# Performance work log

Hardware: AMD Instinct MI355X
Metric: run time of the kernel (lower is better)

Reference implementation:

```python
import jax, jax.numpy as jnp
import numpy as np


def setup_inputs() -> dict:
    key = jax.random.key(0)
    ks = jax.random.split(key, 10)
    B, L, H, E, D = 2, 2048, 16, 64, 64
    d_model = 512
    inp = {
        "queries": jax.random.normal(ks[0], (B, L, H, E), jnp.float32),
        "keys": jax.random.normal(ks[1], (B, L, H, E), jnp.float32),
        "values": jax.random.normal(ks[2], (B, L, H, D), jnp.float32),
        "raw_series": jax.random.normal(ks[3], (B, L, d_model), jnp.float32),
        # learned fusion MLP: Linear(d_model, d_model//2) -> ReLU -> Linear(d_model//2, 1)
        "w1": jax.random.normal(ks[4], (d_model, d_model // 2), jnp.float32) / np.sqrt(d_model),
        "b1": jnp.zeros((d_model // 2,), jnp.float32),
        "w2": jax.random.normal(ks[5], (d_model // 2, 1), jnp.float32) / np.sqrt(d_model // 2),
        "b2": jnp.zeros((1,), jnp.float32),
        # per-head trend scaling, init ones
        "alpha_trend": jnp.ones((H,), jnp.float32),
    }
    return inp


MOMENTUM_ALPHA = 1.0
MOMENTUM_K = 1


def reference(queries, keys, values, raw_series, w1, b1, w2, b2, alpha_trend):
    B, L, H, E = queries.shape
    scale = 1.0 / jnp.sqrt(jnp.asarray(E, queries.dtype))

    # ---- soft momentum bias ----
    # learned fusion: MLP over features -> scalar per position, [B, L]
    h = jax.nn.relu(raw_series @ w1 + b1)
    fused = (h @ w2 + b2)[..., 0]                       # [B, L]
    k = max(1, min(MOMENTUM_K, L - 1))
    momentum = fused[:, k:] - fused[:, :-k]              # [B, L-k]
    momentum = jnp.pad(momentum, ((0, 0), (k, 0)))       # left-pad zeros -> [B, L]
    diff = jnp.abs(momentum[:, :, None] - momentum[:, None, :])  # [B, L, L]
    soft_bias = -MOMENTUM_ALPHA * diff                   # [B, L, L]

    # ---- attention ----
    scores = jnp.einsum('blhe,bshe->bhls', queries, keys)  # [B, H, L, L]
    scores = scores + soft_bias[:, None, :, :] * alpha_trend[None, :, None, None]
    causal = jnp.triu(jnp.ones((L, L), bool), k=1)       # True above diagonal
    scores = jnp.where(causal[None, None], -jnp.inf, scores)
    A = jax.nn.softmax(scale * scores, axis=-1)          # [B, H, L, L]
    V = jnp.einsum('bhls,bshd->blhd', A, values)         # [B, L, H, D]
    return V
```

## Files before the change

### kernel.cpp

```cpp
#include <hip/hip_runtime.h>
#include <math.h>

#define B_ 2
#define L_ 2048
#define H_ 16
#define E_ 64
#define D_ 64
#define DM_ 512
#define DH_ 256

typedef __bf16 bf16_t;
typedef bf16_t bf16x8_t __attribute__((ext_vector_type(8)));
typedef float f32x4_t __attribute__((ext_vector_type(4)));

__device__ __forceinline__ unsigned bpack(float hi, float lo) {
    unsigned uh = __float_as_uint(hi) + 0x8000u;
    unsigned ul = __float_as_uint(lo) + 0x8000u;
    return __builtin_amdgcn_perm(uh, ul, 0x07060302u);
}

__device__ __forceinline__ bf16_t to_bf16(float f) {
    union { float f; unsigned u; } x; x.f = f;
    unsigned r = (x.u + 0x7fffu + ((x.u >> 16) & 1u)) >> 16;
    union { unsigned short s; bf16_t b; } y; y.s = (unsigned short)r;
    return y.b;
}

__device__ __forceinline__ void gload_lds16(const bf16_t* g, bf16_t* l) {
    __builtin_amdgcn_global_load_lds(
        (const __attribute__((address_space(1))) unsigned int*)g,
        (__attribute__((address_space(3))) unsigned int*)l, 16, 0, 0);
}

__device__ __forceinline__ int permK(int sl) {
    return (sl & 3) | (((sl >> 3) & 1) << 2) | (((sl >> 4) & 1) << 3)
         | (((sl >> 2) & 1) << 4) | (((sl >> 5) & 1) << 5);
}

__global__ __launch_bounds__(256) void prep_kernel(
        const float* __restrict__ w1, bf16_t* __restrict__ w1t,
        const float* __restrict__ K, bf16_t* __restrict__ Kp,
        const float* __restrict__ V, bf16_t* __restrict__ Vs,
        float* __restrict__ fused) {
    __shared__ bf16_t T[64][88];
    const int bidx = blockIdx.x;
    const int t = threadIdx.x;

    if (bidx < 256) {
        const int n = bidx;
        #pragma unroll
        for (int u = 0; u < 2; ++u) {
            int k = t + u * 256;
            w1t[(size_t)n * DM_ + k] = to_bf16(w1[(size_t)k * DH_ + n]);
        }
        if (bidx == 0) {
            #pragma unroll
            for (int u = 0; u < 16; ++u) fused[t + u * 256] = 0.f;
        }
        return;
    }

    if (bidx < 1280) {
        const int idx = bidx - 256;
        const int bh = idx >> 5, tile = idx & 31;
        const int b = bh >> 4, h = bh & 15;
        const int sl = t >> 2, e0 = (t & 3) << 4;
        const float* src = K + (((size_t)b * L_ + tile * 64 + sl) * H_ + h) * E_ + e0;
        f32x4_t v0 = *(const f32x4_t*)(src);
        f32x4_t v1 = *(const f32x4_t*)(src + 4);
        f32x4_t v2 = *(const f32x4_t*)(src + 8);
        f32x4_t v3 = *(const f32x4_t*)(src + 12);
        uint4 lo, hi;
        lo.x = bpack(v0[1], v0[0]); lo.y = bpack(v0[3], v0[2]);
        lo.z = bpack(v1[1], v1[0]); lo.w = bpack(v1[3], v1[2]);
        hi.x = bpack(v2[1], v2[0]); hi.y = bpack(v2[3], v2[2]);
        hi.z = bpack(v3[1], v3[0]); hi.w = bpack(v3[3], v3[2]);
        const int r = permK(sl);
        const int bb = r & 7;
        bf16_t* drow = Kp + ((size_t)(bh * 32 + tile) * 64 + r) * 64;
        *(uint4*)(drow + ((((e0 >> 3)    ) ^ bb) << 3)) = lo;
        *(uint4*)(drow + ((((e0 >> 3) + 1) ^ bb) << 3)) = hi;
        return;
    }

    {
        const int idx = bidx - 1280;
        const int bh = idx >> 5, tile = idx & 31;
        const int b = bh >> 4, h = bh & 15;
        const int sl = t >> 2, d0 = (t & 3) << 4;
        const float* src = V + (((size_t)b * L_ + tile * 64 + sl) * H_ + h) * D_ + d0;
        f32x4_t v0 = *(const f32x4_t*)(src);
        f32x4_t v1 = *(const f32x4_t*)(src + 4);
        f32x4_t v2 = *(const f32x4_t*)(src + 8);
        f32x4_t v3 = *(const f32x4_t*)(src + 12);
        uint4 lo, hi;
        lo.x = bpack(v0[1], v0[0]); lo.y = bpack(v0[3], v0[2]);
        lo.z = bpack(v1[1], v1[0]); lo.w = bpack(v1[3], v1[2]);
        hi.x = bpack(v2[1], v2[0]); hi.y = bpack(v2[3], v2[2]);
        hi.z = bpack(v3[1], v3[0]); hi.w = bpack(v3[3], v3[2]);
        *(uint4*)&T[sl][d0]     = lo;
        *(uint4*)&T[sl][d0 + 8] = hi;
        __syncthreads();
        const int d = t & 63, bd = d & 7;
        bf16_t* drow = Vs + ((size_t)bh * 64 + d) * 2048 + tile * 64;
        #pragma unroll
        for (int gg = 0; gg < 2; ++gg) {
            int qb = (t >> 6) + gg * 4;
            int slb = (qb ^ bd) << 3;
            union { unsigned short u[8]; uint4 q; } acc;
            #pragma unroll
            for (int j = 0; j < 8; ++j) {
                union { bf16_t b; unsigned short s; } x; x.b = T[slb + j][d];
                acc.u[j] = x.s;
            }
            *(uint4*)(drow + qb * 8) = acc.q;
        }
    }
}

__global__ __launch_bounds__(256) void mlp_kernel(
        const float* __restrict__ raw, const bf16_t* __restrict__ w1t,
        const float* __restrict__ b1, const float* __restrict__ w2,
        float* __restrict__ fused) {
    __shared__ bf16_t Rs[16][520];
    __shared__ float part[4][16];
    const int t = threadIdx.x;
    const int m0 = (blockIdx.x >> 2) * 16;
    const int nq = blockIdx.x & 3;
    #pragma unroll
    for (int u = 0; u < 8; ++u) {
        int idx = t + u * 256;
        int row = idx >> 7;
        int k = (idx & 127) << 2;
        f32x4_t v = *(const f32x4_t*)&raw[(size_t)(m0 + row) * DM_ + k];
        uint2 p;
        p.x = bpack(v[1], v[0]);
        p.y = bpack(v[3], v[2]);
        *(uint2*)&Rs[row][k] = p;
    }
    __syncthreads();
    const int wave = t >> 6;
    const int lane = t & 63;
    const int lrow = lane & 15;
    const int lgrp = lane >> 4;
    const int n = nq * 64 + wave * 16 + lrow;

    f32x4_t acc = (f32x4_t){0.f, 0.f, 0.f, 0.f};
    const bf16_t* wbase = w1t + (size_t)n * DM_ + lgrp * 8;
    #pragma unroll
    for (int s = 0; s < 16; ++s) {
        bf16x8_t a = *(const bf16x8_t*)&Rs[lrow][s * 32 + lgrp * 8];
        bf16x8_t b = *(const bf16x8_t*)(wbase + s * 32);
        acc = __builtin_amdgcn_mfma_f32_16x16x32_bf16(a, b, acc, 0, 0, 0);
    }
    const float b1v = b1[n];
    const float w2v = w2[n];
    float rowpart[4];
    #pragma unroll
    for (int r = 0; r < 4; ++r) {
        float h = acc[r] + b1v;
        h = h > 0.f ? h : 0.f;
        rowpart[r] = h * w2v;
    }
    #pragma unroll
    for (int r = 0; r < 4; ++r) {
        float v = rowpart[r];
        v += __shfl_xor(v, 1);
        v += __shfl_xor(v, 2);
        v += __shfl_xor(v, 4);
        v += __shfl_xor(v, 8);
        if (lrow == 0) part[wave][lgrp * 4 + r] = v;
    }
    __syncthreads();
    if (t < 16)
        atomicAdd(&fused[m0 + t], part[0][t] + part[1][t] + part[2][t] + part[3][t]);
}

__global__ __launch_bounds__(256) void attn_kernel(
        const float* __restrict__ Q, const bf16_t* __restrict__ Kp,
        const bf16_t* __restrict__ Vs, const float* __restrict__ fused,
        const float* __restrict__ alpha_trend, float* __restrict__ out) {
    __shared__ __align__(16) bf16_t Ks[2][128][64];
    __shared__ __align__(16) bf16_t Vt[2][128][64];
    __shared__ __align__(16) float moms_all[2048];

    const int bid = blockIdx.x;
    const int bh  = bid & 31;
    const int grp = bid >> 5;
    const int qt  = (grp & 1) ? (grp >> 1) : 31 - (grp >> 1);
    const int h = bh & 15, b = bh >> 4;
    const int q0 = qt << 6;
    const int npairs = (qt + 2) >> 1;
    const int tid = threadIdx.x;
    const int wave = tid >> 6, lane = tid & 63;
    const int lrow = lane & 15, lgrp = lane >> 4;

    const float c1 = 0.18033688f;
    const float ascale2 = alpha_trend[h] * c1;
    const size_t bl = (size_t)b * L_;
    const int qw0 = q0 + wave * 16;

    const bf16_t* Kb = Kp + (size_t)bh * 131072;
    const bf16_t* Vb = Vs + (size_t)bh * 131072;
    const float* fusedp = fused + bl;

    #pragma unroll
    for (int u = 0; u < 8; ++u) {
        int i = tid + u * 256;
        float f = fusedp[i];
        float fm = (i == 0) ? f : fusedp[i - 1];
        moms_all[i] = f - fm;
    }

    bf16x8_t a_lo, a_hi;
    {
        const float* qp = Q + ((bl + qw0 + lrow) * H_ + h) * E_ + lgrp * 8;
        f32x4_t v0 = *(const f32x4_t*)(qp);
        f32x4_t v1 = *(const f32x4_t*)(qp + 4);
        f32x4_t v2 = *(const f32x4_t*)(qp + 32);
        f32x4_t v3 = *(const f32x4_t*)(qp + 36);
        #pragma unroll
        for (int k = 0; k < 4; ++k) {
            a_lo[k]     = to_bf16(v0[k] * c1);
            a_lo[4 + k] = to_bf16(v1[k] * c1);
            a_hi[k]     = to_bf16(v2[k] * c1);
            a_hi[4 + k] = to_bf16(v3[k] * c1);
        }
    }
    const int qg = qw0 + lrow;
    const float mq = (qg == 0) ? 0.f : fusedp[qg] - fusedp[qg - 1];

    const bf16_t* ksrc = Kb + wave * 512 + lane * 8;
    const bf16_t* vsrc = Vb + (size_t)(wave * 8 + (lane >> 3)) * 2048 + (lane & 7) * 8;

    f32x4_t Oacc[4];
    #pragma unroll
    for (int c = 0; c < 4; ++c) Oacc[c] = (f32x4_t){0.f, 0.f, 0.f, 0.f};
    float rowsum = 0.f;

    auto stage = [&](int p) {
        const int nb = p & 1;
        const bf16_t* kp0 = ksrc + (size_t)p * 8192;
        gload_lds16(kp0,        &Ks[nb][wave * 8][0]);
        gload_lds16(kp0 + 2048, &Ks[nb][wave * 8 + 32][0]);
        gload_lds16(kp0 + 4096, &Ks[nb][64 + wave * 8][0]);
        gload_lds16(kp0 + 6144, &Ks[nb][64 + wave * 8 + 32][0]);
        const bf16_t* vp0 = vsrc + p * 128;
        gload_lds16(vp0,                  &Vt[nb][wave * 8][0]);
        gload_lds16(vp0 + 32 * 2048,      &Vt[nb][wave * 8 + 32][0]);
        gload_lds16(vp0 + 64,             &Vt[nb][64 + wave * 8][0]);
        gload_lds16(vp0 + 64 + 32 * 2048, &Vt[nb][64 + wave * 8 + 32][0]);
    };

    stage(0);
    for (int p = 0; p < npairs; ++p) {
        __syncthreads();
        if (p + 1 < npairs) stage(p + 1);
        const int nb = p & 1;
        const int bb = lrow & 7;

        #pragma unroll
        for (int sub = 0; sub < 2; ++sub) {
            const int tile = 2 * p + sub;
            const int s0 = tile << 6;
            if (s0 > qw0) continue;

            const char* ksb = (const char*)&Ks[nb][sub * 64][0];
            const char* vtb = (const char*)&Vt[nb][sub * 64][0];

            f32x4_t Sacc[4];
            #pragma unroll
            for (int c = 0; c < 4; ++c) Sacc[c] = (f32x4_t){0.f, 0.f, 0.f, 0.f};
            __builtin_amdgcn_s_setprio(1);
            #pragma unroll
            for (int c = 0; c < 4; ++c) {
                const char* kr = ksb + (c * 16 + lrow) * 128;
                bf16x8_t k_lo = *(const bf16x8_t*)(kr + ((lgrp ^ bb) << 4));
                bf16x8_t k_hi = *(const bf16x8_t*)(kr + (((4 + lgrp) ^ bb) << 4));
                Sacc[c] = __builtin_amdgcn_mfma_f32_16x16x32_bf16(k_lo, a_lo, Sacc[c], 0, 0, 0);
                Sacc[c] = __builtin_amdgcn_mfma_f32_16x16x32_bf16(k_hi, a_hi, Sacc[c], 0, 0, 0);
            }
            __builtin_amdgcn_s_setprio(0);

            float rowe[4][4];
            #pragma unroll
            for (int c = 0; c < 4; ++c) {
                const int sb = lgrp * 8 + ((c & 1) << 2) + ((c >> 1) << 5);
                f32x4_t ms4 = *(const f32x4_t*)&moms_all[s0 + sb];
                #pragma unroll
                for (int r = 0; r < 4; ++r) {
                    float arg = Sacc[c][r] - ascale2 * fabsf(mq - ms4[r]);
                    rowe[c][r] = __builtin_amdgcn_exp2f(arg);
                }
            }
            if (tile == qt) {
                #pragma unroll
                for (int c = 0; c < 4; ++c) {
                    const int sg0 = s0 + lgrp * 8 + ((c & 1) << 2) + ((c >> 1) << 5);
                    #pragma unroll
                    for (int r = 0; r < 4; ++r)
                        if (sg0 + r > qg) rowe[c][r] = 0.f;
                }
            }
            #pragma unroll
            for (int c = 0; c < 4; ++c)
                rowsum += (rowe[c][0] + rowe[c][1]) + (rowe[c][2] + rowe[c][3]);

            #pragma unroll
            for (int hh = 0; hh < 2; ++hh) {
                union { unsigned u[4]; bf16x8_t v; } pa;
                pa.u[0] = bpack(rowe[2 * hh][1],     rowe[2 * hh][0]);
                pa.u[1] = bpack(rowe[2 * hh][3],     rowe[2 * hh][2]);
                pa.u[2] = bpack(rowe[2 * hh + 1][1], rowe[2 * hh + 1][0]);
                pa.u[3] = bpack(rowe[2 * hh + 1][3], rowe[2 * hh + 1][2]);
                __builtin_amdgcn_s_setprio(1);
                #pragma unroll
                for (int c2 = 0; c2 < 4; ++c2) {
                    const int row = c2 * 16 + lrow;
                    bf16x8_t bv = *(const bf16x8_t*)(vtb + row * 128 +
                                                     (((hh * 4 + lgrp) ^ bb) << 4));
                    Oacc[c2] = __builtin_amdgcn_mfma_f32_16x16x32_bf16(pa.v, bv, Oacc[c2], 0, 0, 0);
                }
                __builtin_amdgcn_s_setprio(0);
            }
        }
    }

    float rs = rowsum;
    rs += __shfl_xor(rs, 16);
    rs += __shfl_xor(rs, 32);
    #pragma unroll
    for (int r = 0; r < 4; ++r) {
        float inv = 1.f / __shfl(rs, lgrp * 4 + r);
        size_t orow = ((bl + qw0 + lgrp * 4 + r) * H_ + h) * D_;
        #pragma unroll
        for (int c = 0; c < 4; ++c)
            out[orow + c * 16 + lrow] = Oacc[c][r] * inv;
    }
}

extern "C" void kernel_launch(void* const* d_in, const int* in_sizes, int n_in,
                              void* d_out, int out_size, void* d_ws, size_t ws_size,
                              hipStream_t stream) {
    const float* Q     = (const float*)d_in[0];
    const float* K     = (const float*)d_in[1];
    const float* V     = (const float*)d_in[2];
    const float* raw   = (const float*)d_in[3];
    const float* w1    = (const float*)d_in[4];
    const float* b1    = (const float*)d_in[5];
    const float* w2    = (const float*)d_in[6];
    const float* alpha = (const float*)d_in[8];
    float* out = (float*)d_out;

    float* fused = (float*)d_ws;
    bf16_t* w1t  = (bf16_t*)(fused + B_ * L_);
    bf16_t* Kp   = w1t + 256 * 512;
    bf16_t* Vs   = Kp + (size_t)B_ * H_ * L_ * E_;

    prep_kernel<<<2304, 256, 0, stream>>>(w1, w1t, K, Kp, V, Vs, fused);
    mlp_kernel<<<B_ * L_ / 16 * 4, 256, 0, stream>>>(raw, w1t, b1, w2, fused);
    attn_kernel<<<B_ * H_ * (L_ / 64), 256, 0, stream>>>(Q, Kp, Vs, fused, alpha, out);
}
```

Measured before the change: 169.6 us.

## Merge MLP into prep kernel and replace atomics with per-quarter partial sums

Folds the fused-MLP computation into the K/V conversion kernel, which drops one kernel launch and the separate w1 transpose-to-bf16 pass. MLP blocks now read fp32 w1 directly with strided column loads and convert in-register. Instead of atomically accumulating into a zeroed buffer, each of the four N-quarters writes its own partial, and the attention kernel sums the four partials when computing momentum. This removes the zero-init dependency and the atomics, at the cost of uncoalesced w1 reads and extra loads in attention.

```diff
diff --git a/kernel.cpp b/kernel.cpp
--- a/kernel.cpp
+++ b/kernel.cpp
@@ -37,32 +37,21 @@
          | (((sl >> 2) & 1) << 4) | (((sl >> 5) & 1) << 5);
 }
 
-__global__ __launch_bounds__(256) void prep_kernel(
-        const float* __restrict__ w1, bf16_t* __restrict__ w1t,
+__global__ __launch_bounds__(256) void prep_mlp_kernel(
         const float* __restrict__ K, bf16_t* __restrict__ Kp,
         const float* __restrict__ V, bf16_t* __restrict__ Vs,
-        float* __restrict__ fused) {
-    __shared__ bf16_t T[64][88];
+        const float* __restrict__ raw, const float* __restrict__ w1,
+        const float* __restrict__ b1, const float* __restrict__ w2,
+        float* __restrict__ fused4) {
+    __shared__ union {
+        bf16_t T[64][88];
+        struct { bf16_t Rs[16][520]; float part[4][16]; } m;
+    } S;
     const int bidx = blockIdx.x;
     const int t = threadIdx.x;
 
-    if (bidx < 256) {
-        const int n = bidx;
-        #pragma unroll
-        for (int u = 0; u < 2; ++u) {
-            int k = t + u * 256;
-            w1t[(size_t)n * DM_ + k] = to_bf16(w1[(size_t)k * DH_ + n]);
-        }
-        if (bidx == 0) {
-            #pragma unroll
-            for (int u = 0; u < 16; ++u) fused[t + u * 256] = 0.f;
-        }
-        return;
-    }
-
-    if (bidx < 1280) {
-        const int idx = bidx - 256;
-        const int bh = idx >> 5, tile = idx & 31;
+    if (bidx < 1024) {
+        const int bh = bidx >> 5, tile = bidx & 31;
         const int b = bh >> 4, h = bh & 15;
         const int sl = t >> 2, e0 = (t & 3) << 4;
         const float* src = K + (((size_t)b * L_ + tile * 64 + sl) * H_ + h) * E_ + e0;
@@ -83,8 +72,8 @@
         return;
     }
 
-    {
-        const int idx = bidx - 1280;
+    if (bidx < 2048) {
+        const int idx = bidx - 1024;
         const int bh = idx >> 5, tile = idx & 31;
         const int b = bh >> 4, h = bh & 15;
         const int sl = t >> 2, d0 = (t & 3) << 4;
@@ -98,8 +87,8 @@
         lo.z = bpack(v1[1], v1[0]); lo.w = bpack(v1[3], v1[2]);
         hi.x = bpack(v2[1], v2[0]); hi.y = bpack(v2[3], v2[2]);
         hi.z = bpack(v3[1], v3[0]); hi.w = bpack(v3[3], v3[2]);
-        *(uint4*)&T[sl][d0]     = lo;
-        *(uint4*)&T[sl][d0 + 8] = hi;
+        *(uint4*)&S.T[sl][d0]     = lo;
+        *(uint4*)&S.T[sl][d0 + 8] = hi;
         __syncthreads();
         const int d = t & 63, bd = d & 7;
         bf16_t* drow = Vs + ((size_t)bh * 64 + d) * 2048 + tile * 64;
@@ -110,75 +99,75 @@
             union { unsigned short u[8]; uint4 q; } acc;
             #pragma unroll
             for (int j = 0; j < 8; ++j) {
-                union { bf16_t b; unsigned short s; } x; x.b = T[slb + j][d];
+                union { bf16_t b; unsigned short s; } x; x.b = S.T[slb + j][d];
                 acc.u[j] = x.s;
             }
             *(uint4*)(drow + qb * 8) = acc.q;
         }
-    }
-}
-
-__global__ __launch_bounds__(256) void mlp_kernel(
-        const float* __restrict__ raw, const bf16_t* __restrict__ w1t,
-        const float* __restrict__ b1, const float* __restrict__ w2,
-        float* __restrict__ fused) {
-    __shared__ bf16_t Rs[16][520];
-    __shared__ float part[4][16];
-    const int t = threadIdx.x;
-    const int m0 = (blockIdx.x >> 2) * 16;
-    const int nq = blockIdx.x & 3;
-    #pragma unroll
-    for (int u = 0; u < 8; ++u) {
-        int idx = t + u * 256;
-        int row = idx >> 7;
-        int k = (idx & 127) << 2;
-        f32x4_t v = *(const f32x4_t*)&raw[(size_t)(m0 + row) * DM_ + k];
-        uint2 p;
-        p.x = bpack(v[1], v[0]);
-        p.y = bpack(v[3], v[2]);
-        *(uint2*)&Rs[row][k] = p;
-    }
-    __syncthreads();
-    const int wave = t >> 6;
-    const int lane = t & 63;
-    const int lrow = lane & 15;
-    const int lgrp = lane >> 4;
-    const int n = nq * 64 + wave * 16 + lrow;
-
-    f32x4_t acc = (f32x4_t){0.f, 0.f, 0.f, 0.f};
-    const bf16_t* wbase = w1t + (size_t)n * DM_ + lgrp * 8;
-    #pragma unroll
-    for (int s = 0; s < 16; ++s) {
-        bf16x8_t a = *(const bf16x8_t*)&Rs[lrow][s * 32 + lgrp * 8];
-        bf16x8_t b = *(const bf16x8_t*)(wbase + s * 32);
-        acc = __builtin_amdgcn_mfma_f32_16x16x32_bf16(a, b, acc, 0, 0, 0);
-    }
-    const float b1v = b1[n];
-    const float w2v = w2[n];
-    float rowpart[4];
-    #pragma unroll
-    for (int r = 0; r < 4; ++r) {
-        float h = acc[r] + b1v;
-        h = h > 0.f ? h : 0.f;
-        rowpart[r] = h * w2v;
-    }
-    #pragma unroll
-    for (int r = 0; r < 4; ++r) {
-        float v = rowpart[r];
-        v += __shfl_xor(v, 1);
-        v += __shfl_xor(v, 2);
-        v += __shfl_xor(v, 4);
-        v += __shfl_xor(v, 8);
-        if (lrow == 0) part[wave][lgrp * 4 + r] = v;
-    }
-    __syncthreads();
-    if (t < 16)
-        atomicAdd(&fused[m0 + t], part[0][t] + part[1][t] + part[2][t] + part[3][t]);
+        return;
+    }
+
+    {
+        const int mb = bidx - 2048;
+        const int m0 = (mb >> 2) * 16;
+        const int nq = mb & 3;
+        #pragma unroll
+        for (int u = 0; u < 8; ++u) {
+            int idx = t + u * 256;
+            int row = idx >> 7;
+            int k = (idx & 127) << 2;
+            f32x4_t v = *(const f32x4_t*)&raw[(size_t)(m0 + row) * DM_ + k];
+            uint2 p;
+            p.x = bpack(v[1], v[0]);
+            p.y = bpack(v[3], v[2]);
+            *(uint2*)&S.m.Rs[row][k] = p;
+        }
+        __syncthreads();
+        const int wave = t >> 6;
+        const int lane = t & 63;
+        const int lrow = lane & 15;
+        const int lgrp = lane >> 4;
+        const int n = nq * 64 + wave * 16 + lrow;
+
+        f32x4_t acc = (f32x4_t){0.f, 0.f, 0.f, 0.f};
+        const float* wcol = w1 + n;
+        #pragma unroll
+        for (int s = 0; s < 16; ++s) {
+            bf16x8_t a = *(const bf16x8_t*)&S.m.Rs[lrow][s * 32 + lgrp * 8];
+            const float* wp = wcol + (size_t)(s * 32 + lgrp * 8) * DH_;
+            bf16x8_t bfr;
+            #pragma unroll
+            for (int j = 0; j < 8; ++j) bfr[j] = to_bf16(wp[(size_t)j * DH_]);
+            acc = __builtin_amdgcn_mfma_f32_16x16x32_bf16(a, bfr, acc, 0, 0, 0);
+        }
+        const float b1v = b1[n];
+        const float w2v = w2[n];
+        float rowpart[4];
+        #pragma unroll
+        for (int r = 0; r < 4; ++r) {
+            float h = acc[r] + b1v;
+            h = h > 0.f ? h : 0.f;
+            rowpart[r] = h * w2v;
+        }
+        #pragma unroll
+        for (int r = 0; r < 4; ++r) {
+            float v = rowpart[r];
+            v += __shfl_xor(v, 1);
+            v += __shfl_xor(v, 2);
+            v += __shfl_xor(v, 4);
+            v += __shfl_xor(v, 8);
+            if (lrow == 0) S.m.part[wave][lgrp * 4 + r] = v;
+        }
+        __syncthreads();
+        if (t < 16)
+            fused4[nq * (B_ * L_) + m0 + t] =
+                S.m.part[0][t] + S.m.part[1][t] + S.m.part[2][t] + S.m.part[3][t];
+    }
 }
 
 __global__ __launch_bounds__(256) void attn_kernel(
         const float* __restrict__ Q, const bf16_t* __restrict__ Kp,
-        const bf16_t* __restrict__ Vs, const float* __restrict__ fused,
+        const bf16_t* __restrict__ Vs, const float* __restrict__ fused4,
         const float* __restrict__ alpha_trend, float* __restrict__ out) {
     __shared__ __align__(16) bf16_t Ks[2][128][64];
     __shared__ __align__(16) bf16_t Vt[2][128][64];
@@ -202,14 +191,18 @@
 
     const bf16_t* Kb = Kp + (size_t)bh * 131072;
     const bf16_t* Vb = Vs + (size_t)bh * 131072;
-    const float* fusedp = fused + bl;
+    const float* f4 = fused4 + bl;
 
     #pragma unroll
     for (int u = 0; u < 8; ++u) {
         int i = tid + u * 256;
-        float f = fusedp[i];
-        float fm = (i == 0) ? f : fusedp[i - 1];
-        moms_all[i] = f - fm;
+        float mv = 0.f;
+        if (i > 0) {
+            float f0 = f4[i]     + f4[4096 + i]     + f4[8192 + i]     + f4[12288 + i];
+            float fm = f4[i - 1] + f4[4096 + i - 1] + f4[8192 + i - 1] + f4[12288 + i - 1];
+            mv = f0 - fm;
+        }
+        moms_all[i] = mv;
     }
 
     bf16x8_t a_lo, a_hi;
@@ -228,7 +221,12 @@
         }
     }
     const int qg = qw0 + lrow;
-    const float mq = (qg == 0) ? 0.f : fusedp[qg] - fusedp[qg - 1];
+    float mq = 0.f;
+    if (qg > 0) {
+        float f0 = f4[qg]     + f4[4096 + qg]     + f4[8192 + qg]     + f4[12288 + qg];
+        float fm = f4[qg - 1] + f4[4096 + qg - 1] + f4[8192 + qg - 1] + f4[12288 + qg - 1];
+        mq = f0 - fm;
+    }
 
     const bf16_t* ksrc = Kb + wave * 512 + lane * 8;
     const bf16_t* vsrc = Vb + (size_t)(wave * 8 + (lane >> 3)) * 2048 + (lane & 7) * 8;
@@ -352,12 +350,10 @@
     const float* alpha = (const float*)d_in[8];
     float* out = (float*)d_out;
 
-    float* fused = (float*)d_ws;
-    bf16_t* w1t  = (bf16_t*)(fused + B_ * L_);
-    bf16_t* Kp   = w1t + 256 * 512;
-    bf16_t* Vs   = Kp + (size_t)B_ * H_ * L_ * E_;
-
-    prep_kernel<<<2304, 256, 0, stream>>>(w1, w1t, K, Kp, V, Vs, fused);
-    mlp_kernel<<<B_ * L_ / 16 * 4, 256, 0, stream>>>(raw, w1t, b1, w2, fused);
-    attn_kernel<<<B_ * H_ * (L_ / 64), 256, 0, stream>>>(Q, Kp, Vs, fused, alpha, out);
-}
+    float* fused4 = (float*)d_ws;
+    bf16_t* Kp    = (bf16_t*)(fused4 + 4 * B_ * L_);
+    bf16_t* Vs    = Kp + (size_t)B_ * H_ * L_ * E_;
+
+    prep_mlp_kernel<<<3072, 256, 0, stream>>>(K, Kp, V, Vs, raw, w1, b1, w2, fused4);
+    attn_kernel<<<B_ * H_ * (L_ / 64), 256, 0, stream>>>(Q, Kp, Vs, fused4, alpha, out);
+}
```

New measurement: 167.0 us. No clear change (-1.5%).
